# Optimization experiments

Hardware: AMD Instinct MI355X
Metric: run time of the kernel (lower is better)

The kernel has to match this reference:

```python
import jax, jax.numpy as jnp
import numpy as np

GRID_NUM = 28
IMG_SIZE = 224.0
GRID_SIZE = IMG_SIZE / GRID_NUM
LAMBDA_COORD = 5.0
LAMBDA_NOOBJ = 0.5
NUM_CLASSES = 20
EPS = 1e-12


def setup_inputs() -> dict:
    key = jax.random.key(0)
    k1, k2, k3 = jax.random.split(key, 3)
    B, S = 1024, GRID_NUM
    y_pred = jax.random.uniform(k1, (B, S, S, 30), dtype=jnp.float32)
    # y_true channel 0: class id in {0..20}; 0 means no object. channels 1:5: (x, y, w, h)
    cls = jax.random.randint(k2, (B, S, S, 1), 0, NUM_CLASSES + 1).astype(jnp.float32)
    box = jax.random.uniform(k3, (B, S, S, 4), dtype=jnp.float32)
    y_true = jnp.concatenate([cls, box], axis=-1)
    return {"y_pred": y_pred, "y_true": y_true}


def _corners(box, gi, gj):
    # box[..., 0:2] are cell-relative center offsets, box[..., 2:4] are image-relative w/h
    cx = (gj + box[..., 0]) * GRID_SIZE
    cy = (gi + box[..., 1]) * GRID_SIZE
    w = box[..., 2] * IMG_SIZE
    h = box[..., 3] * IMG_SIZE
    return cx - w / 2, cy - h / 2, cx + w / 2, cy + h / 2


def _iou(box_a, box_b, gi, gj):
    ax1, ay1, ax2, ay2 = _corners(box_a, gi, gj)
    bx1, by1, bx2, by2 = _corners(box_b, gi, gj)
    iw = jnp.maximum(jnp.minimum(ax2, bx2) - jnp.maximum(ax1, bx1), 0.0)
    ih = jnp.maximum(jnp.minimum(ay2, by2) - jnp.maximum(ay1, by1), 0.0)
    inter = iw * ih
    area_a = jnp.maximum(ax2 - ax1, 0.0) * jnp.maximum(ay2 - ay1, 0.0)
    area_b = jnp.maximum(bx2 - bx1, 0.0) * jnp.maximum(by2 - by1, 0.0)
    return inter / (area_a + area_b - inter + EPS)


def reference(y_pred, y_true):
    B, S = y_pred.shape[0], y_pred.shape[1]
    gi = jnp.arange(S, dtype=jnp.float32)[None, :, None]  # broadcast over (B, S, S)
    gj = jnp.arange(S, dtype=jnp.float32)[None, None, :]

    obj_mask = y_true[..., 0] != 0.0  # (B, S, S)
    true_box = y_true[..., 1:5]

    iou0 = _iou(y_pred[..., 0:4], true_box, gi, gj)
    iou1 = _iou(y_pred[..., 5:9], true_box, gi, gj)
    # original: choose 0 iff iou0 > iou1, else 1
    choose1 = ~(iou0 > iou1)

    conf_pred = jnp.where(choose1, y_pred[..., 9], y_pred[..., 4])
    conf_true = jnp.where(choose1, iou1, iou0)
    xy_pred = jnp.where(choose1[..., None], y_pred[..., 5:7], y_pred[..., 0:2])

    loss_conf_obj = jnp.square(conf_pred - conf_true)
    loss_coord = LAMBDA_COORD * jnp.sum(jnp.square(xy_pred - y_true[..., 1:3]), axis=-1)

    cls_idx = y_true[..., 0].astype(jnp.int32) - 1
    cls_onehot = jax.nn.one_hot(cls_idx, NUM_CLASSES, dtype=y_pred.dtype)
    loss_cls = jnp.sum(jnp.square(y_pred[..., 10:] - cls_onehot), axis=-1)

    loss_conf_noobj = LAMBDA_NOOBJ * (jnp.square(y_pred[..., 4]) + jnp.square(y_pred[..., 9]))

    bsz = jnp.float32(B)
    loss_confidence = jnp.sum(jnp.where(obj_mask, loss_conf_obj, loss_conf_noobj)) / bsz
    loss_coordinate = jnp.sum(jnp.where(obj_mask, loss_coord, 0.0)) / bsz
    loss_classification = jnp.sum(jnp.where(obj_mask, loss_cls, 0.0)) / bsz
    return loss_confidence + loss_coordinate + loss_classification
```

## Files before the change

### kernel.cpp

```cpp
#include <hip/hip_runtime.h>


#define S_GRID 28
#define N_CELLS (1024 * S_GRID * S_GRID)
#define CPW 64
#define N_TILES (N_CELLS / CPW)
#define WPB 2
#define BLOCK (WPB * 64)
#define NBLOCKS 1024
#define NWAVES (NBLOCKS * WPB)

typedef unsigned int u32;

__device__ __forceinline__ void async16(const float* g, float* l) {
    __builtin_amdgcn_global_load_lds((const __attribute__((address_space(1))) u32*)g,
                                     (__attribute__((address_space(3))) u32*)l, 16, 0, 0);
}
__device__ __forceinline__ void async4(const float* g, float* l) {
    __builtin_amdgcn_global_load_lds((const __attribute__((address_space(1))) u32*)g,
                                     (__attribute__((address_space(3))) u32*)l, 4, 0, 0);
}

__device__ __forceinline__ void stage(const float* __restrict__ yp,
                                      const float* __restrict__ yt,
                                      int tile, int lane,
                                      float* spred, float* syt) {
    const float* gp = yp + (size_t)tile * (CPW * 30);
#pragma unroll
    for (int j = 0; j < 7; ++j)
        async16(gp + j * 256 + lane * 4, spred + j * 256);
    async4(gp + 1792 + lane, spred + 1792);
    async4(gp + 1856 + lane, spred + 1856);
    const float* gt = yt + (size_t)tile * (CPW * 5);
#pragma unroll
    for (int j = 0; j < 5; ++j)
        async4(gt + j * 64 + lane, syt + j * 64);
}

__device__ __forceinline__ float iou_calc(float bx, float by, float bw, float bh,
                                          float tx, float ty, float tw, float th,
                                          float gi, float gj) {
    float acx = (gj + bx) * 8.0f;
    float acy = (gi + by) * 8.0f;
    float aw  = bw * 224.0f;
    float ah  = bh * 224.0f;
    float ax1 = acx - aw * 0.5f, ax2 = acx + aw * 0.5f;
    float ay1 = acy - ah * 0.5f, ay2 = acy + ah * 0.5f;
    float bcx = (gj + tx) * 8.0f;
    float bcy = (gi + ty) * 8.0f;
    float btw = tw * 224.0f;
    float bth = th * 224.0f;
    float bx1 = bcx - btw * 0.5f, bx2 = bcx + btw * 0.5f;
    float by1 = bcy - bth * 0.5f, by2 = bcy + bth * 0.5f;

    float iw = fmaxf(fminf(ax2, bx2) - fmaxf(ax1, bx1), 0.0f);
    float ih = fmaxf(fminf(ay2, by2) - fmaxf(ay1, by1), 0.0f);
    float inter = iw * ih;
    float area_a = fmaxf(ax2 - ax1, 0.0f) * fmaxf(ay2 - ay1, 0.0f);
    float area_b = fmaxf(bx2 - bx1, 0.0f) * fmaxf(by2 - by1, 0.0f);
    return inter / (area_a + area_b - inter + 1e-12f);
}

__global__ __launch_bounds__(BLOCK, 2) void yolo_loss_kernel(const float* __restrict__ yp,
                                                             const float* __restrict__ yt,
                                                             float* __restrict__ partials) {
    __shared__ __align__(16) float sp[WPB][2][CPW * 30];
    __shared__ __align__(16) float sy[WPB][2][CPW * 5];

    int tid  = threadIdx.x;
    int lane = tid & 63;
    int wave = tid >> 6;
    int gwave = blockIdx.x * WPB + wave;

    float acc = 0.0f;
    int buf = 0;

    stage(yp, yt, gwave, lane, sp[wave][0], sy[wave][0]);

    for (int t = gwave; t < N_TILES; t += NWAVES) {
        int tn = t + NWAVES;
        if (tn < N_TILES) {
            stage(yp, yt, tn, lane, sp[wave][buf ^ 1], sy[wave][buf ^ 1]);
            asm volatile("s_waitcnt vmcnt(14)" ::: "memory");
        } else {
            asm volatile("s_waitcnt vmcnt(0)" ::: "memory");
        }

        const float* spw = sp[wave][buf];
        const float* syw = sy[wave][buf];

        const float2* p2 = (const float2*)(spw + lane * 30);
        float pr[30];
#pragma unroll
        for (int k = 0; k < 15; ++k) {
            float2 q = p2[k];
            pr[2 * k]     = q.x;
            pr[2 * k + 1] = q.y;
        }
        float tc = syw[lane * 5 + 0];
        float tx = syw[lane * 5 + 1];
        float ty = syw[lane * 5 + 2];
        float tw = syw[lane * 5 + 3];
        float th = syw[lane * 5 + 4];

        int cell = t * CPW + lane;
        int ij = cell % (S_GRID * S_GRID);
        float gi = (float)(ij / S_GRID);
        float gj = (float)(ij % S_GRID);

        float iou0 = iou_calc(pr[0], pr[1], pr[2], pr[3], tx, ty, tw, th, gi, gj);
        float iou1 = iou_calc(pr[5], pr[6], pr[7], pr[8], tx, ty, tw, th, gi, gj);
        bool choose1 = !(iou0 > iou1);

        float conf_pred = choose1 ? pr[9] : pr[4];
        float conf_true = choose1 ? iou1 : iou0;
        float xp  = choose1 ? pr[5] : pr[0];
        float ypv = choose1 ? pr[6] : pr[1];

        float dcf = conf_pred - conf_true;
        float d0 = xp - tx, d1 = ypv - ty;

        int cls = (int)tc - 1;
        float lcls = 0.0f;
#pragma unroll
        for (int k = 0; k < 20; ++k) {
            float oh = (k == cls) ? 1.0f : 0.0f;
            float d = pr[10 + k] - oh;
            lcls += d * d;
        }

        float obj_loss   = dcf * dcf + 5.0f * (d0 * d0 + d1 * d1) + lcls;
        float noobj_loss = 0.5f * (pr[4] * pr[4] + pr[9] * pr[9]);
        acc += (tc != 0.0f) ? obj_loss : noobj_loss;

        buf ^= 1;
    }

#pragma unroll
    for (int off = 32; off > 0; off >>= 1) {
        acc += __shfl_down(acc, off, 64);
    }
    if (lane == 0) partials[gwave] = acc;
}

__global__ __launch_bounds__(256) void reduce_kernel(const float* __restrict__ partials,
                                                     float* __restrict__ out) {
    int tid = threadIdx.x;
    float s = 0.0f;
#pragma unroll
    for (int k = 0; k < 8; ++k) {
        s += partials[k * 256 + tid];
    }
#pragma unroll
    for (int off = 32; off > 0; off >>= 1) {
        s += __shfl_down(s, off, 64);
    }
    __shared__ float wsum[4];
    int lane = tid & 63;
    int wid  = tid >> 6;
    if (lane == 0) wsum[wid] = s;
    __syncthreads();
    if (tid == 0) {
        out[0] = (wsum[0] + wsum[1] + wsum[2] + wsum[3]) * (1.0f / 1024.0f);
    }
}

extern "C" void kernel_launch(void* const* d_in, const int* in_sizes, int n_in,
                              void* d_out, int out_size, void* d_ws, size_t ws_size,
                              hipStream_t stream) {
    const float* y_pred = (const float*)d_in[0];
    const float* y_true = (const float*)d_in[1];
    float* out = (float*)d_out;
    float* partials = (float*)d_ws;

    yolo_loss_kernel<<<NBLOCKS, BLOCK, 0, stream>>>(y_pred, y_true, partials);
    reduce_kernel<<<1, 256, 0, stream>>>(partials, out);
}
```

Measured before the change: 153.3 us.

## Replace async global-to-LDS loads with register-staged prefetch and LDS transpose

Drops the global_load_lds direct-to-LDS path. Each wave now loads the next tile into registers with coalesced vector loads while it computes the current tile, then writes those registers into the alternate LDS buffer after the compute. y_true is read straight into registers per lane and no longer goes through LDS. The grid grows to 1280 blocks and the reduce kernel is adjusted to match. This uses more registers and adds explicit LDS writes, in exchange for letting the compiler schedule the loads and avoiding the hand-written vmcnt waits.

```diff
diff --git a/kernel.cpp b/kernel.cpp
--- a/kernel.cpp
+++ b/kernel.cpp
@@ -7,35 +7,12 @@
 #define N_TILES (N_CELLS / CPW)
 #define WPB 2
 #define BLOCK (WPB * 64)
-#define NBLOCKS 1024
+#define NBLOCKS 1280
 #define NWAVES (NBLOCKS * WPB)
+#define PRED_FLOATS (CPW * 30)
 
-typedef unsigned int u32;
-
-__device__ __forceinline__ void async16(const float* g, float* l) {
-    __builtin_amdgcn_global_load_lds((const __attribute__((address_space(1))) u32*)g,
-                                     (__attribute__((address_space(3))) u32*)l, 16, 0, 0);
-}
-__device__ __forceinline__ void async4(const float* g, float* l) {
-    __builtin_amdgcn_global_load_lds((const __attribute__((address_space(1))) u32*)g,
-                                     (__attribute__((address_space(3))) u32*)l, 4, 0, 0);
-}
-
-__device__ __forceinline__ void stage(const float* __restrict__ yp,
-                                      const float* __restrict__ yt,
-                                      int tile, int lane,
-                                      float* spred, float* syt) {
-    const float* gp = yp + (size_t)tile * (CPW * 30);
-#pragma unroll
-    for (int j = 0; j < 7; ++j)
-        async16(gp + j * 256 + lane * 4, spred + j * 256);
-    async4(gp + 1792 + lane, spred + 1792);
-    async4(gp + 1856 + lane, spred + 1856);
-    const float* gt = yt + (size_t)tile * (CPW * 5);
-#pragma unroll
-    for (int j = 0; j < 5; ++j)
-        async4(gt + j * 64 + lane, syt + j * 64);
-}
+typedef float v4f __attribute__((ext_vector_type(4)));
+typedef float v2f __attribute__((ext_vector_type(2)));
 
 __device__ __forceinline__ float iou_calc(float bx, float by, float bw, float bh,
                                           float tx, float ty, float tw, float th,
@@ -64,8 +41,7 @@
 __global__ __launch_bounds__(BLOCK, 2) void yolo_loss_kernel(const float* __restrict__ yp,
                                                              const float* __restrict__ yt,
                                                              float* __restrict__ partials) {
-    __shared__ __align__(16) float sp[WPB][2][CPW * 30];
-    __shared__ __align__(16) float sy[WPB][2][CPW * 5];
+    __shared__ __align__(16) float lds[WPB][2][PRED_FLOATS];
 
     int tid  = threadIdx.x;
     int lane = tid & 63;
@@ -73,35 +49,53 @@
     int gwave = blockIdx.x * WPB + wave;
 
     float acc = 0.0f;
-    int buf = 0;
+    int cur = 0;
 
-    stage(yp, yt, gwave, lane, sp[wave][0], sy[wave][0]);
+    v4f a0, a1, a2, a3, a4, a5, a6;
+    v2f a7;
+    float b0, b1, b2, b3, b4;
+    float tc, tx, ty, tw, th;
+
+    {
+        const v4f* g4 = (const v4f*)(yp + (size_t)gwave * PRED_FLOATS);
+        a0 = g4[0 * 64 + lane]; a1 = g4[1 * 64 + lane]; a2 = g4[2 * 64 + lane];
+        a3 = g4[3 * 64 + lane]; a4 = g4[4 * 64 + lane]; a5 = g4[5 * 64 + lane];
+        a6 = g4[6 * 64 + lane];
+        a7 = ((const v2f*)(yp + (size_t)gwave * PRED_FLOATS + 1792))[lane];
+        const float* gt = yt + (size_t)(gwave * CPW + lane) * 5;
+        b0 = gt[0]; b1 = gt[1]; b2 = gt[2]; b3 = gt[3]; b4 = gt[4];
+
+        v4f* s4 = (v4f*)lds[wave][0];
+        s4[0 * 64 + lane] = a0; s4[1 * 64 + lane] = a1; s4[2 * 64 + lane] = a2;
+        s4[3 * 64 + lane] = a3; s4[4 * 64 + lane] = a4; s4[5 * 64 + lane] = a5;
+        s4[6 * 64 + lane] = a6;
+        ((v2f*)(lds[wave][0] + 1792))[lane] = a7;
+        tc = b0; tx = b1; ty = b2; tw = b3; th = b4;
+    }
 
     for (int t = gwave; t < N_TILES; t += NWAVES) {
         int tn = t + NWAVES;
-        if (tn < N_TILES) {
-            stage(yp, yt, tn, lane, sp[wave][buf ^ 1], sy[wave][buf ^ 1]);
-            asm volatile("s_waitcnt vmcnt(14)" ::: "memory");
-        } else {
-            asm volatile("s_waitcnt vmcnt(0)" ::: "memory");
+        bool more = (tn < N_TILES);
+
+        if (more) {
+            const v4f* g4 = (const v4f*)(yp + (size_t)tn * PRED_FLOATS);
+            a0 = g4[0 * 64 + lane]; a1 = g4[1 * 64 + lane]; a2 = g4[2 * 64 + lane];
+            a3 = g4[3 * 64 + lane]; a4 = g4[4 * 64 + lane]; a5 = g4[5 * 64 + lane];
+            a6 = g4[6 * 64 + lane];
+            a7 = ((const v2f*)(yp + (size_t)tn * PRED_FLOATS + 1792))[lane];
+            const float* gt = yt + (size_t)(tn * CPW + lane) * 5;
+            b0 = gt[0]; b1 = gt[1]; b2 = gt[2]; b3 = gt[3]; b4 = gt[4];
         }
+        __builtin_amdgcn_sched_barrier(0);
 
-        const float* spw = sp[wave][buf];
-        const float* syw = sy[wave][buf];
-
-        const float2* p2 = (const float2*)(spw + lane * 30);
+        const float* cp = lds[wave][cur] + lane * 30;
         float pr[30];
 #pragma unroll
         for (int k = 0; k < 15; ++k) {
-            float2 q = p2[k];
+            v2f q = *(const v2f*)(cp + 2 * k);
             pr[2 * k]     = q.x;
             pr[2 * k + 1] = q.y;
         }
-        float tc = syw[lane * 5 + 0];
-        float tx = syw[lane * 5 + 1];
-        float ty = syw[lane * 5 + 2];
-        float tw = syw[lane * 5 + 3];
-        float th = syw[lane * 5 + 4];
 
         int cell = t * CPW + lane;
         int ij = cell % (S_GRID * S_GRID);
@@ -133,7 +127,18 @@
         float noobj_loss = 0.5f * (pr[4] * pr[4] + pr[9] * pr[9]);
         acc += (tc != 0.0f) ? obj_loss : noobj_loss;
 
-        buf ^= 1;
+        __builtin_amdgcn_sched_barrier(0);
+
+        if (more) {
+            float* nb = lds[wave][cur ^ 1];
+            v4f* s4 = (v4f*)nb;
+            s4[0 * 64 + lane] = a0; s4[1 * 64 + lane] = a1; s4[2 * 64 + lane] = a2;
+            s4[3 * 64 + lane] = a3; s4[4 * 64 + lane] = a4; s4[5 * 64 + lane] = a5;
+            s4[6 * 64 + lane] = a6;
+            ((v2f*)(nb + 1792))[lane] = a7;
+            tc = b0; tx = b1; ty = b2; tw = b3; th = b4;
+        }
+        cur ^= 1;
     }
 
 #pragma unroll
@@ -148,7 +153,7 @@
     int tid = threadIdx.x;
     float s = 0.0f;
 #pragma unroll
-    for (int k = 0; k < 8; ++k) {
+    for (int k = 0; k < 10; ++k) {
         s += partials[k * 256 + tid];
     }
 #pragma unroll
```

Measured after the change: 154.4 us. About the same (+0.8%).
